# Kernel optimization log

Hardware: AMD Instinct MI355X
Metric: run time of the kernel (lower is better)

Reference implementation:

```python
import jax, jax.numpy as jnp
import numpy as np

B, N, D, P = 4, 512, 512, 128

def setup_inputs() -> dict:
    key = jax.random.key(0)
    ks = jax.random.split(key, 8)
    s = lambda fan_in: 1.0 / np.sqrt(fan_in)
    inp = {
        "input": jax.random.normal(ks[0], (B, N, D), dtype=jnp.float32),
        # bigram projections (weights stored [in, out]; torch Linear is [out, in])
        "Wl": jax.random.uniform(ks[1], (D, P), jnp.float32, -s(D), s(D)),
        "bl": jnp.zeros((P,), jnp.float32),  # zeroed in initialize_parameters
        "Wr": jax.random.uniform(ks[2], (D, P), jnp.float32, -s(D), s(D)),  # no bias
        "Wo": jax.random.uniform(ks[3], (P, 1), jnp.float32, -s(P), s(P)),
        "bo": jnp.zeros((1,), jnp.float32),
        # start builder MLP
        "Ws1": jax.random.uniform(ks[4], (D, P), jnp.float32, -s(D), s(D)),
        "bs1": jnp.zeros((P,), jnp.float32),
        "Ws2": jax.random.uniform(ks[5], (P, 1), jnp.float32, -s(P), s(P)),
        "bs2": jnp.zeros((1,), jnp.float32),
        # end builder MLP
        "We1": jax.random.uniform(ks[6], (D, P), jnp.float32, -s(D), s(D)),
        "be1": jnp.zeros((P,), jnp.float32),
        "We2": jax.random.uniform(ks[7], (P, 1), jnp.float32, -s(P), s(P)),
        "be2": jnp.zeros((1,), jnp.float32),
    }
    return inp


def reference(input, Wl, bl, Wr, Wo, bo, Ws1, bs1, Ws2, bs2, We1, be1, We2, be2):
    # start / end unigram scores: [B, N, 1]
    start = jnp.maximum(input @ Ws1 + bs1, 0.0) @ Ws2 + bs2
    end = jnp.maximum(input @ We1 + be1, 0.0) @ We2 + be2
    # bigram scores
    left = input @ Wl + bl   # [B, N, P]
    right = input @ Wr       # [B, N, P]
    # left.unsqueeze(1) + right.unsqueeze(2) -> [B, N, N, P]
    proj = left[:, None, :, :] + right[:, :, None, :]
    bigram = jnp.maximum(proj, 0.0) @ Wo + bo  # [B, N, N, 1]
    return (bigram, start, end)
```

## Files before the change

kernel.cpp:

```cpp
#include <hip/hip_runtime.h>

typedef unsigned short ushort_t;
using f32x4  = __attribute__((ext_vector_type(4))) float;
using bf16x8 = __attribute__((ext_vector_type(8))) short;
using u16x8  = __attribute__((ext_vector_type(8))) unsigned short;

constexpr int Bc = 4;
constexpr int Nc = 512;
constexpr int Dc = 512;
constexpr int Pc = 128;
constexpr int ROWS = Bc * Nc;

__device__ inline unsigned short f2bf(float f) {
    unsigned u = __builtin_bit_cast(unsigned, f);
    unsigned r = u + 0x7fffu + ((u >> 16) & 1u);
    return (unsigned short)(r >> 16);
}

__global__ __launch_bounds__(256) void convert_kernel(
    const float* __restrict__ input,
    const float* __restrict__ Wl,  const float* __restrict__ Wr,
    const float* __restrict__ Ws1, const float* __restrict__ We1,
    ushort_t* __restrict__ inBF, ushort_t* __restrict__ WcatT)
{
    const int bx = blockIdx.x, t = threadIdx.x;
    if (bx < 64) {
        const int ct = bx >> 3, kt = bx & 7;
        const int c0 = ct * 64, k0 = kt * 64;
        const int mi = c0 >> 7;
        const float* Wm = (mi == 0) ? Wl : (mi == 1) ? Wr : (mi == 2) ? Ws1 : We1;
        const int cm0 = c0 & 127;

        __shared__ float T[64][68];
        const int kk = t >> 4, cc = (t & 15) << 2;
        #pragma unroll
        for (int u = 0; u < 4; ++u)
            *(float4*)&T[kk + u * 16][cc] =
                *(const float4*)&Wm[(size_t)(k0 + kk + u * 16) * Pc + cm0 + cc];
        __syncthreads();

        const int c_l = t >> 2, kb = (t & 3) << 4;
        u16x8 o0, o1;
        #pragma unroll
        for (int u = 0; u < 8; ++u) o0[u] = f2bf(T[kb + u][c_l]);
        #pragma unroll
        for (int u = 0; u < 8; ++u) o1[u] = f2bf(T[kb + 8 + u][c_l]);
        ushort_t* dst = &WcatT[(size_t)(c0 + c_l) * Dc + k0 + kb];
        *(u16x8*)dst = o0;
        *(u16x8*)(dst + 8) = o1;
    } else {
        const size_t idx0 = (size_t)(bx - 64) * 2048 + (size_t)t * 8;
        float4 v0 = *(const float4*)&input[idx0];
        float4 v1 = *(const float4*)&input[idx0 + 4];
        u16x8 o;
        o[0] = f2bf(v0.x); o[1] = f2bf(v0.y); o[2] = f2bf(v0.z); o[3] = f2bf(v0.w);
        o[4] = f2bf(v1.x); o[5] = f2bf(v1.y); o[6] = f2bf(v1.z); o[7] = f2bf(v1.w);
        *(u16x8*)&inBF[idx0] = o;
    }
}

__device__ inline ushort_t* swz(ushort_t* base, int row, int kbyte) {
    return (ushort_t*)((char*)base + row * 128 + (kbyte ^ ((row & 7) << 4)));
}

__global__ __launch_bounds__(256) void mfma_proj_kernel(
    const ushort_t* __restrict__ inBF, const ushort_t* __restrict__ WcatT,
    const float* __restrict__ bl,
    const float* __restrict__ bs1, const float* __restrict__ Ws2,
    const float* __restrict__ be1, const float* __restrict__ We2,
    float* __restrict__ left, float* __restrict__ right,
    float* __restrict__ parts)
{
    const int mt = blockIdx.x, ny = blockIdx.y;
    const int row0 = mt * 64, col0 = ny * 64;
    const int t = threadIdx.x;
    const int w = t >> 6, l = t & 63;
    const int wm = w >> 1, wn = w & 1;

    __shared__ ushort_t As[64 * 64];
    __shared__ ushort_t Bs[64 * 64];
    __shared__ float red[2][64];

    f32x4 acc[2][2];
    #pragma unroll
    for (int m = 0; m < 2; ++m)
        #pragma unroll
        for (int n = 0; n < 2; ++n)
            acc[m][n] = f32x4{0.f, 0.f, 0.f, 0.f};

    const int sr = t >> 2;
    const int kb0 = (t & 3) << 5;
    const ushort_t* Ag = inBF  + (size_t)(row0 + sr) * Dc + (kb0 >> 1);
    const ushort_t* Bg = WcatT + (size_t)(col0 + sr) * Dc + (kb0 >> 1);

    float4 aR0 = *(const float4*)Ag,       aR1 = *(const float4*)(Ag + 8);
    float4 bR0 = *(const float4*)Bg,       bR1 = *(const float4*)(Bg + 8);

    const int fr = l & 15, fg = l >> 4;

    for (int ks = 0; ks < 8; ++ks) {
        *(float4*)swz(As, sr, kb0)      = aR0;
        *(float4*)swz(As, sr, kb0 + 16) = aR1;
        *(float4*)swz(Bs, sr, kb0)      = bR0;
        *(float4*)swz(Bs, sr, kb0 + 16) = bR1;
        __syncthreads();

        if (ks < 7) {
            const ushort_t* Ag2 = Ag + (ks + 1) * 64;
            const ushort_t* Bg2 = Bg + (ks + 1) * 64;
            aR0 = *(const float4*)Ag2; aR1 = *(const float4*)(Ag2 + 8);
            bR0 = *(const float4*)Bg2; bR1 = *(const float4*)(Bg2 + 8);
        }

        #pragma unroll
        for (int kk = 0; kk < 2; ++kk) {
            bf16x8 a0 = *(bf16x8*)swz(As, wm * 32 + fr,      kk * 64 + fg * 16);
            bf16x8 a1 = *(bf16x8*)swz(As, wm * 32 + 16 + fr, kk * 64 + fg * 16);
            bf16x8 b0 = *(bf16x8*)swz(Bs, wn * 32 + fr,      kk * 64 + fg * 16);
            bf16x8 b1 = *(bf16x8*)swz(Bs, wn * 32 + 16 + fr, kk * 64 + fg * 16);
            acc[0][0] = __builtin_amdgcn_mfma_f32_16x16x32_bf16(a0, b0, acc[0][0], 0, 0, 0);
            acc[0][1] = __builtin_amdgcn_mfma_f32_16x16x32_bf16(a0, b1, acc[0][1], 0, 0, 0);
            acc[1][0] = __builtin_amdgcn_mfma_f32_16x16x32_bf16(a1, b0, acc[1][0], 0, 0, 0);
            acc[1][1] = __builtin_amdgcn_mfma_f32_16x16x32_bf16(a1, b1, acc[1][1], 0, 0, 0);
        }
        __syncthreads();
    }

    const int fq4 = fg << 2;
    if (ny < 4) {
        float* outp = (ny < 2) ? left : right;
        const int cbase = (ny & 1) * 64 + wn * 32;
        #pragma unroll
        for (int m = 0; m < 2; ++m) {
            const int row = row0 + wm * 32 + m * 16 + fq4;
            #pragma unroll
            for (int n = 0; n < 2; ++n) {
                const int col = cbase + n * 16 + fr;
                const float bv = (ny < 2) ? bl[col] : 0.f;
                #pragma unroll
                for (int q = 0; q < 4; ++q)
                    outp[(size_t)(row + q) * Pc + col] = acc[m][n][q] + bv;
            }
        }
    } else {
        const float* b1 = (ny < 6) ? bs1 : be1;
        const float* W2 = (ny < 6) ? Ws2 : We2;
        const int pbase = (ny < 6) ? (ny - 4) * 64 : (ny - 6) * 64;
        float vs[2][4];
        #pragma unroll
        for (int m = 0; m < 2; ++m)
            #pragma unroll
            for (int q = 0; q < 4; ++q) {
                float v = 0.f;
                #pragma unroll
                for (int n = 0; n < 2; ++n) {
                    const int cp = pbase + wn * 32 + n * 16 + fr;
                    v += fmaxf(acc[m][n][q] + b1[cp], 0.f) * W2[cp];
                }
                v += __shfl_xor(v, 1);
                v += __shfl_xor(v, 2);
                v += __shfl_xor(v, 4);
                v += __shfl_xor(v, 8);
                vs[m][q] = v;
            }
        if (fr == 0) {
            #pragma unroll
            for (int m = 0; m < 2; ++m)
                #pragma unroll
                for (int q = 0; q < 4; ++q)
                    red[wn][wm * 32 + m * 16 + fq4 + q] = vs[m][q];
        }
        __syncthreads();
        if (t < 64) {
            const int pi = ny - 4;
            parts[pi * ROWS + row0 + t] = red[0][t] + red[1][t];
        }
    }
}

__global__ __launch_bounds__(256) void bigram_kernel(
    const float* __restrict__ left, const float* __restrict__ right,
    const float* __restrict__ Wo,   const float* __restrict__ bo,
    const float* __restrict__ parts,
    const float* __restrict__ bs2,  const float* __restrict__ be2,
    float* __restrict__ out, float* __restrict__ start_out,
    float* __restrict__ end_out)
{
    const int jt = blockIdx.x, it = blockIdx.y, b = blockIdx.z;
    const int t  = threadIdx.x;

    if (jt == 8) {
        if (it >= 8) return;
        const int base = (b * 8 + it) * 64;
        if (t < 64) {
            const int r = base + t;
            start_out[r] = parts[r] + parts[ROWS + r] + bs2[0];
        } else if (t < 128) {
            const int r = base + t - 64;
            end_out[r] = parts[2 * ROWS + r] + parts[3 * ROWS + r] + be2[0];
        }
        return;
    }

    __shared__ float Ls[64][132];
    __shared__ float Rs[32][132];
    __shared__ float wos[Pc];

    const float* lp = left  + (size_t)(b * Nc + jt * 64) * Pc;
    const float* rp = right + (size_t)(b * Nc + it * 32) * Pc;

    #pragma unroll
    for (int u = 0; u < 8; ++u) {
        int f = t + u * 256, r = f >> 5, p4 = (f & 31) << 2;
        *(float4*)&Ls[r][p4] = *(const float4*)&lp[r * Pc + p4];
    }
    #pragma unroll
    for (int u = 0; u < 4; ++u) {
        int f = t + u * 256, r = f >> 5, p4 = (f & 31) << 2;
        *(float4*)&Rs[r][p4] = *(const float4*)&rp[r * Pc + p4];
    }
    if (t < 32) *(float4*)&wos[t << 2] = *(const float4*)&Wo[t << 2];
    __syncthreads();

    const int jl = t & 15;
    const int il = t >> 4;

    float acc[2][4] = {};

#define LOADG(P, W4, L4, R4)                                             \
    {                                                                    \
        W4 = *(const float4*)&wos[(P)];                                  \
        _Pragma("unroll") for (int jj = 0; jj < 4; ++jj)                 \
            L4[jj] = *(const float4*)&Ls[jl + 16 * jj][(P)];             \
        _Pragma("unroll") for (int ii = 0; ii < 2; ++ii)                 \
            R4[ii] = *(const float4*)&Rs[il + 16 * ii][(P)];             \
    }

#define COMPUTE(W4, L4, R4)                                              \
    {                                                                    \
        _Pragma("unroll") for (int ii = 0; ii < 2; ++ii)                 \
        _Pragma("unroll") for (int jj = 0; jj < 4; ++jj) {               \
            acc[ii][jj] = fmaf(fmaxf(L4[jj].x + R4[ii].x, 0.f), W4.x, acc[ii][jj]); \
            acc[ii][jj] = fmaf(fmaxf(L4[jj].y + R4[ii].y, 0.f), W4.y, acc[ii][jj]); \
            acc[ii][jj] = fmaf(fmaxf(L4[jj].z + R4[ii].z, 0.f), W4.z, acc[ii][jj]); \
            acc[ii][jj] = fmaf(fmaxf(L4[jj].w + R4[ii].w, 0.f), W4.w, acc[ii][jj]); \
        }                                                                \
    }

    float4 wa, la[4], ra[2];
    float4 wb, lb4[4], rb4[2];
    LOADG(0, wa, la, ra);

    #pragma unroll 1
    for (int p = 0; p < Pc; p += 8) {
        LOADG(p + 4, wb, lb4, rb4);
        COMPUTE(wa, la, ra);
        if (p + 8 < Pc) LOADG(p + 8, wa, la, ra);
        COMPUTE(wb, lb4, rb4);
    }

    const float bias = bo[0];
    #pragma unroll
    for (int ii = 0; ii < 2; ++ii) {
        #pragma unroll
        for (int jj = 0; jj < 4; ++jj) {
            const int gi = it * 32 + il + 16 * ii;
            const int gj = jt * 64 + jl + 16 * jj;
            out[((size_t)b * Nc + gi) * Nc + gj] = acc[ii][jj] + bias;
        }
    }
#undef LOADG
#undef COMPUTE
}

extern "C" void kernel_launch(void* const* d_in, const int* in_sizes, int n_in,
                              void* d_out, int out_size, void* d_ws, size_t ws_size,
                              hipStream_t stream) {
    const float* input = (const float*)d_in[0];
    const float* Wl  = (const float*)d_in[1];
    const float* bl  = (const float*)d_in[2];
    const float* Wr  = (const float*)d_in[3];
    const float* Wo  = (const float*)d_in[4];
    const float* bo  = (const float*)d_in[5];
    const float* Ws1 = (const float*)d_in[6];
    const float* bs1 = (const float*)d_in[7];
    const float* Ws2 = (const float*)d_in[8];
    const float* bs2 = (const float*)d_in[9];
    const float* We1 = (const float*)d_in[10];
    const float* be1 = (const float*)d_in[11];
    const float* We2 = (const float*)d_in[12];
    const float* be2 = (const float*)d_in[13];

    float* out    = (float*)d_out;
    float* bigram = out;
    float* start  = out + (size_t)Bc * Nc * Nc;
    float* end    = start + (size_t)Bc * Nc;

    float* left   = (float*)d_ws;
    float* right  = left + (size_t)ROWS * Pc;
    float* parts  = right + (size_t)ROWS * Pc;
    ushort_t* inBF  = (ushort_t*)(parts + 4 * ROWS);
    ushort_t* WcatT = inBF + (size_t)ROWS * Dc;

    convert_kernel<<<576, 256, 0, stream>>>(input, Wl, Wr, Ws1, We1, inBF, WcatT);

    mfma_proj_kernel<<<dim3(32, 8), 256, 0, stream>>>(
        inBF, WcatT, bl, bs1, Ws2, be1, We2, left, right, parts);

    bigram_kernel<<<dim3(9, 16, 4), 256, 0, stream>>>(
        left, right, Wo, bo, parts, bs2, be2, bigram, start, end);
}
```

Before: 37.66 us.

## Pre-tile bf16 operands and stage projection GEMM via direct global-to-LDS loads

The convert kernel now writes the bf16 input and transposed weights in a tile-blocked, k-chunk-major layout. That layout lets the projection GEMM copy each 64x64 tile straight from global memory into LDS using global_load_lds, with no register round-trip or swizzle. The GEMM also double-buffers LDS so the next k-slice loads while the current one computes. The change adds LDS usage, and without a swizzle the fragment reads may hit LDS bank conflicts. The bigram kernel dominates total time, so the overall effect may be limited.

Result: no change. 38.18 us (+1.4%).

```diff
diff --git a/kernel.cpp b/kernel.cpp
--- a/kernel.cpp
+++ b/kernel.cpp
@@ -17,54 +17,64 @@
     return (unsigned short)(r >> 16);
 }
 
+__device__ inline void gload_lds16(const void* g, void* l) {
+    __builtin_amdgcn_global_load_lds(
+        (const __attribute__((address_space(1))) unsigned int*)g,
+        (__attribute__((address_space(3))) unsigned int*)l, 16, 0, 0);
+}
+
 __global__ __launch_bounds__(256) void convert_kernel(
     const float* __restrict__ input,
     const float* __restrict__ Wl,  const float* __restrict__ Wr,
     const float* __restrict__ Ws1, const float* __restrict__ We1,
-    ushort_t* __restrict__ inBF, ushort_t* __restrict__ WcatT)
+    ushort_t* __restrict__ inBF2, ushort_t* __restrict__ WcatT2)
 {
     const int bx = blockIdx.x, t = threadIdx.x;
-    if (bx < 64) {
-        const int ct = bx >> 3, kt = bx & 7;
-        const int c0 = ct * 64, k0 = kt * 64;
-        const int mi = c0 >> 7;
+    __shared__ float T[64][68];
+
+    if (bx < 256) {
+        const int mt = bx >> 3, ks = bx & 7;
+        const int c = t & 7, r0 = t >> 3;
+        const float* src = input + (size_t)(mt * 64) * Dc + ks * 64;
+        ushort_t* dstc = inBF2 + ((size_t)(mt * 8 + ks) * 8 + c) * 512;
+        #pragma unroll
+        for (int h = 0; h < 2; ++h) {
+            const int r = r0 + h * 32;
+            const float* s = src + (size_t)r * Dc + c * 8;
+            float4 v0 = *(const float4*)s;
+            float4 v1 = *(const float4*)(s + 4);
+            u16x8 o;
+            o[0] = f2bf(v0.x); o[1] = f2bf(v0.y); o[2] = f2bf(v0.z); o[3] = f2bf(v0.w);
+            o[4] = f2bf(v1.x); o[5] = f2bf(v1.y); o[6] = f2bf(v1.z); o[7] = f2bf(v1.w);
+            *(u16x8*)(dstc + r * 8) = o;
+        }
+    } else {
+        const int idx = bx - 256;
+        const int nt = idx >> 3, ks = idx & 7;
+        const int mi = nt >> 1, cm0 = (nt & 1) * 64;
         const float* Wm = (mi == 0) ? Wl : (mi == 1) ? Wr : (mi == 2) ? Ws1 : We1;
-        const int cm0 = c0 & 127;
-
-        __shared__ float T[64][68];
-        const int kk = t >> 4, cc = (t & 15) << 2;
+
+        const int kk_ = t >> 4, cc = (t & 15) << 2;
         #pragma unroll
         for (int u = 0; u < 4; ++u)
-            *(float4*)&T[kk + u * 16][cc] =
-                *(const float4*)&Wm[(size_t)(k0 + kk + u * 16) * Pc + cm0 + cc];
+            *(float4*)&T[kk_ + 16 * u][cc] =
+                *(const float4*)&Wm[(size_t)(ks * 64 + kk_ + 16 * u) * Pc + cm0 + cc];
         __syncthreads();
 
-        const int c_l = t >> 2, kb = (t & 3) << 4;
-        u16x8 o0, o1;
-        #pragma unroll
-        for (int u = 0; u < 8; ++u) o0[u] = f2bf(T[kb + u][c_l]);
-        #pragma unroll
-        for (int u = 0; u < 8; ++u) o1[u] = f2bf(T[kb + 8 + u][c_l]);
-        ushort_t* dst = &WcatT[(size_t)(c0 + c_l) * Dc + k0 + kb];
-        *(u16x8*)dst = o0;
-        *(u16x8*)(dst + 8) = o1;
-    } else {
-        const size_t idx0 = (size_t)(bx - 64) * 2048 + (size_t)t * 8;
-        float4 v0 = *(const float4*)&input[idx0];
-        float4 v1 = *(const float4*)&input[idx0 + 4];
-        u16x8 o;
-        o[0] = f2bf(v0.x); o[1] = f2bf(v0.y); o[2] = f2bf(v0.z); o[3] = f2bf(v0.w);
-        o[4] = f2bf(v1.x); o[5] = f2bf(v1.y); o[6] = f2bf(v1.z); o[7] = f2bf(v1.w);
-        *(u16x8*)&inBF[idx0] = o;
-    }
-}
-
-__device__ inline ushort_t* swz(ushort_t* base, int row, int kbyte) {
-    return (ushort_t*)((char*)base + row * 128 + (kbyte ^ ((row & 7) << 4)));
-}
-
-__global__ __launch_bounds__(256) void mfma_proj_kernel(
-    const ushort_t* __restrict__ inBF, const ushort_t* __restrict__ WcatT,
+        const int col = t & 63, c2 = t >> 6;
+        #pragma unroll
+        for (int h = 0; h < 2; ++h) {
+            const int kc = c2 + h * 4;
+            u16x8 o;
+            #pragma unroll
+            for (int i = 0; i < 8; ++i) o[i] = f2bf(T[kc * 8 + i][col]);
+            *(u16x8*)(WcatT2 + ((size_t)(nt * 8 + ks) * 8 + kc) * 512 + col * 8) = o;
+        }
+    }
+}
+
+__global__ __launch_bounds__(256) void mfma_proj2(
+    const ushort_t* __restrict__ inBF2, const ushort_t* __restrict__ WcatT2,
     const float* __restrict__ bl,
     const float* __restrict__ bs1, const float* __restrict__ Ws2,
     const float* __restrict__ be1, const float* __restrict__ We2,
@@ -72,14 +82,17 @@
     float* __restrict__ parts)
 {
     const int mt = blockIdx.x, ny = blockIdx.y;
-    const int row0 = mt * 64, col0 = ny * 64;
-    const int t = threadIdx.x;
-    const int w = t >> 6, l = t & 63;
+    const int row0 = mt * 64;
+    const int t = threadIdx.x, w = t >> 6, l = t & 63;
     const int wm = w >> 1, wn = w & 1;
-
-    __shared__ ushort_t As[64 * 64];
-    __shared__ ushort_t Bs[64 * 64];
+    const int fr = l & 15, fg = l >> 4;
+
+    __shared__ ushort_t As2[2][4096];
+    __shared__ ushort_t Bs2[2][4096];
     __shared__ float red[2][64];
+
+    const ushort_t* Abase = inBF2  + (size_t)mt * 8 * 4096;
+    const ushort_t* Bbase = WcatT2 + (size_t)ny * 8 * 4096;
 
     f32x4 acc[2][2];
     #pragma unroll
@@ -88,36 +101,31 @@
         for (int n = 0; n < 2; ++n)
             acc[m][n] = f32x4{0.f, 0.f, 0.f, 0.f};
 
-    const int sr = t >> 2;
-    const int kb0 = (t & 3) << 5;
-    const ushort_t* Ag = inBF  + (size_t)(row0 + sr) * Dc + (kb0 >> 1);
-    const ushort_t* Bg = WcatT + (size_t)(col0 + sr) * Dc + (kb0 >> 1);
-
-    float4 aR0 = *(const float4*)Ag,       aR1 = *(const float4*)(Ag + 8);
-    float4 bR0 = *(const float4*)Bg,       bR1 = *(const float4*)(Bg + 8);
-
-    const int fr = l & 15, fg = l >> 4;
+    const int c0 = 2 * w, c1 = 2 * w + 1;
+
+#define STAGE(BI, KS)                                                        \
+    {                                                                        \
+        const ushort_t* ga = Abase + (KS) * 4096;                            \
+        const ushort_t* gb = Bbase + (KS) * 4096;                            \
+        gload_lds16(ga + c0 * 512 + l * 8, &As2[BI][c0 * 512]);              \
+        gload_lds16(ga + c1 * 512 + l * 8, &As2[BI][c1 * 512]);              \
+        gload_lds16(gb + c0 * 512 + l * 8, &Bs2[BI][c0 * 512]);              \
+        gload_lds16(gb + c1 * 512 + l * 8, &Bs2[BI][c1 * 512]);              \
+    }
+
+    STAGE(0, 0);
+    __syncthreads();
 
     for (int ks = 0; ks < 8; ++ks) {
-        *(float4*)swz(As, sr, kb0)      = aR0;
-        *(float4*)swz(As, sr, kb0 + 16) = aR1;
-        *(float4*)swz(Bs, sr, kb0)      = bR0;
-        *(float4*)swz(Bs, sr, kb0 + 16) = bR1;
-        __syncthreads();
-
-        if (ks < 7) {
-            const ushort_t* Ag2 = Ag + (ks + 1) * 64;
-            const ushort_t* Bg2 = Bg + (ks + 1) * 64;
-            aR0 = *(const float4*)Ag2; aR1 = *(const float4*)(Ag2 + 8);
-            bR0 = *(const float4*)Bg2; bR1 = *(const float4*)(Bg2 + 8);
-        }
-
+        const int bi = ks & 1;
+        if (ks < 7) STAGE(bi ^ 1, ks + 1);
         #pragma unroll
         for (int kk = 0; kk < 2; ++kk) {
-            bf16x8 a0 = *(bf16x8*)swz(As, wm * 32 + fr,      kk * 64 + fg * 16);
-            bf16x8 a1 = *(bf16x8*)swz(As, wm * 32 + 16 + fr, kk * 64 + fg * 16);
-            bf16x8 b0 = *(bf16x8*)swz(Bs, wn * 32 + fr,      kk * 64 + fg * 16);
-            bf16x8 b1 = *(bf16x8*)swz(Bs, wn * 32 + 16 + fr, kk * 64 + fg * 16);
+            const int kc = kk * 4 + fg;
+            bf16x8 a0 = *(const bf16x8*)&As2[bi][(kc * 64 + wm * 32 + fr) * 8];
+            bf16x8 a1 = *(const bf16x8*)&As2[bi][(kc * 64 + wm * 32 + 16 + fr) * 8];
+            bf16x8 b0 = *(const bf16x8*)&Bs2[bi][(kc * 64 + wn * 32 + fr) * 8];
+            bf16x8 b1 = *(const bf16x8*)&Bs2[bi][(kc * 64 + wn * 32 + 16 + fr) * 8];
             acc[0][0] = __builtin_amdgcn_mfma_f32_16x16x32_bf16(a0, b0, acc[0][0], 0, 0, 0);
             acc[0][1] = __builtin_amdgcn_mfma_f32_16x16x32_bf16(a0, b1, acc[0][1], 0, 0, 0);
             acc[1][0] = __builtin_amdgcn_mfma_f32_16x16x32_bf16(a1, b0, acc[1][0], 0, 0, 0);
@@ -125,6 +133,7 @@
         }
         __syncthreads();
     }
+#undef STAGE
 
     const int fq4 = fg << 2;
     if (ny < 4) {
@@ -299,13 +308,13 @@
     float* left   = (float*)d_ws;
     float* right  = left + (size_t)ROWS * Pc;
     float* parts  = right + (size_t)ROWS * Pc;
-    ushort_t* inBF  = (ushort_t*)(parts + 4 * ROWS);
-    ushort_t* WcatT = inBF + (size_t)ROWS * Dc;
-
-    convert_kernel<<<576, 256, 0, stream>>>(input, Wl, Wr, Ws1, We1, inBF, WcatT);
-
-    mfma_proj_kernel<<<dim3(32, 8), 256, 0, stream>>>(
-        inBF, WcatT, bl, bs1, Ws2, be1, We2, left, right, parts);
+    ushort_t* inBF2  = (ushort_t*)(parts + 4 * ROWS);
+    ushort_t* WcatT2 = inBF2 + (size_t)ROWS * Dc;
+
+    convert_kernel<<<320, 256, 0, stream>>>(input, Wl, Wr, Ws1, We1, inBF2, WcatT2);
+
+    mfma_proj2<<<dim3(32, 8), 256, 0, stream>>>(
+        inBF2, WcatT2, bl, bs1, Ws2, be1, We2, left, right, parts);
 
     bigram_kernel<<<dim3(9, 16, 4), 256, 0, stream>>>(
         left, right, Wo, bo, parts, bs2, be2, bigram, start, end);
```
